# Performance work log

Hardware: AMD Instinct MI355X
Metric: run time of the kernel (lower is better)

Reference implementation:

```python
import jax, jax.numpy as jnp
import numpy as np

B, N, C, H = 4, 1024, 1024, 16
HD = C // H
SCALE = HD ** -0.5


def _init_linear(key, out_dim, in_dim):
    # torch nn.Linear default init: U(-1/sqrt(in), 1/sqrt(in)) for weight and bias
    kw, kb = jax.random.split(key)
    bound = 1.0 / np.sqrt(in_dim)
    W = jax.random.uniform(kw, (out_dim, in_dim), jnp.float32, -bound, bound)
    b = jax.random.uniform(kb, (out_dim,), jnp.float32, -bound, bound)
    return W, b


def setup_inputs() -> dict:
    key = jax.random.key(0)
    ks = jax.random.split(key, 5)
    x = jax.random.normal(ks[0], (B, N, C), jnp.float32)
    # NdLinear qkv: Linear(N->N) along seq axis, then Linear(C->3C) along channel axis
    Wq0, bq0 = _init_linear(ks[1], N, N)
    Wq1, bq1 = _init_linear(ks[2], 3 * C, C)
    # NdLinear proj: Linear(N->N) along seq axis, then Linear(C->C) along channel axis
    Wp0, bp0 = _init_linear(ks[3], N, N)
    Wp1, bp1 = _init_linear(ks[4], C, C)
    return {"x": x, "Wq0": Wq0, "bq0": bq0, "Wq1": Wq1, "bq1": bq1,
            "Wp0": Wp0, "bp0": bp0, "Wp1": Wp1, "bp1": bp1}


def _ndlinear(x, W0, b0, W1, b1):
    # NdLinear over (seq, channel): apply Linear along axis 1, then axis 2.
    # torch Linear: y = x @ W.T + b
    x = jnp.einsum('bnc,mn->bmc', x, W0) + b0[None, :, None]   # seq axis
    x = jnp.einsum('bnc,dc->bnd', x, W1) + b1                  # channel axis
    return x


def reference(x, Wq0, bq0, Wq1, bq1, Wp0, bp0, Wp1, bp1):
    qkv = _ndlinear(x, Wq0, bq0, Wq1, bq1)                     # (B, N, 3C)
    qkv = qkv.reshape(B, N, 3, H, HD).transpose(2, 0, 3, 1, 4) # (3, B, H, N, HD)
    q, k, v = qkv[0], qkv[1], qkv[2]
    attn = jnp.einsum('bhnd,bhmd->bhnm', q, k) * SCALE         # (B, H, N, N)
    attn = jax.nn.softmax(attn, axis=-1)
    out = jnp.einsum('bhnm,bhmd->bhnd', attn, v)               # (B, H, N, HD)
    out = out.transpose(0, 2, 1, 3).reshape(B, N, C)
    out = _ndlinear(out, Wp0, bp0, Wp1, bp1)
    return out
```

## Files before the change

### kernel.cpp

```cpp
#include <hip/hip_runtime.h>
#include <hip/hip_bf16.h>
#include <stdint.h>

typedef __bf16 bf16;
typedef __bf16 bf16x4 __attribute__((ext_vector_type(4)));
typedef __bf16 bf16x8 __attribute__((ext_vector_type(8)));
typedef float f32x4 __attribute__((ext_vector_type(4)));

#define B_ 4
#define N_ 1024
#define C_ 1024
#define H_ 16
#define MEG (1u << 20)

__device__ __forceinline__ uint32_t lds_off(const void* p) {
    return (uint32_t)(uintptr_t)p;
}
__device__ __forceinline__ void g2l16(const void* g, uint32_t lds_byte) {
    __builtin_amdgcn_global_load_lds(
        (const __attribute__((address_space(1))) unsigned int*)(uintptr_t)g,
        (__attribute__((address_space(3))) unsigned int*)(uintptr_t)lds_byte,
        16, 0, 0);
}

__global__ __launch_bounds__(256) void prep_k(
    const float* __restrict__ x, bf16* __restrict__ xT,
    const float* __restrict__ s0, bf16* __restrict__ d0,
    const float* __restrict__ s1, bf16* __restrict__ d1,
    const float* __restrict__ s2, bf16* __restrict__ d2,
    const float* __restrict__ s3, bf16* __restrict__ d3)
{
    __shared__ bf16 t[64][66];
    const int bid = blockIdx.x;
    const int tid = threadIdx.x;
    if (bid < 3072) {
        const float* s; bf16* d; int base;
        if (bid < 512)       { s = s0; d = d0; base = 0; }
        else if (bid < 2048) { s = s1; d = d1; base = 512; }
        else if (bid < 2560) { s = s2; d = d2; base = 2048; }
        else                 { s = s3; d = d3; base = 2560; }
        int i = ((bid - base) * 256 + tid) * 8;
        float4 a = *(const float4*)(s + i);
        float4 b = *(const float4*)(s + i + 4);
        bf16x8 r;
        r[0] = (bf16)a.x; r[1] = (bf16)a.y; r[2] = (bf16)a.z; r[3] = (bf16)a.w;
        r[4] = (bf16)b.x; r[5] = (bf16)b.y; r[6] = (bf16)b.z; r[7] = (bf16)b.w;
        *(bf16x8*)(d + i) = r;
        return;
    }
    const int idx = bid - 3072;
    const int c0 = (idx & 15) * 64, n0 = ((idx >> 4) & 15) * 64, b = idx >> 8;
    {
        int nl = tid >> 2, seg = tid & 3;
        const float* src = x + ((size_t)b * N_ + n0 + nl) * C_ + c0 + seg * 16;
#pragma unroll
        for (int i = 0; i < 4; ++i) {
            float4 v = *(const float4*)(src + i * 4);
            t[nl][seg * 16 + i * 4 + 0] = (bf16)v.x;
            t[nl][seg * 16 + i * 4 + 1] = (bf16)v.y;
            t[nl][seg * 16 + i * 4 + 2] = (bf16)v.z;
            t[nl][seg * 16 + i * 4 + 3] = (bf16)v.w;
        }
    }
    __syncthreads();
    {
        int cl = tid >> 2, seg = tid & 3;
        bf16* dst = xT + ((size_t)b * C_ + c0 + cl) * N_ + n0 + seg * 16;
        bf16x8 o0, o1;
#pragma unroll
        for (int j = 0; j < 8; ++j) o0[j] = t[seg * 16 + j][cl];
#pragma unroll
        for (int j = 0; j < 8; ++j) o1[j] = t[seg * 16 + 8 + j][cl];
        *(bf16x8*)dst = o0;
        *(bf16x8*)(dst + 8) = o1;
    }
}

template <int BIAS, bool OF32, bool VSPLIT>
__global__ __launch_bounds__(512) void gemm_k(
    const bf16* __restrict__ A, const bf16* __restrict__ Bm,
    const float* __restrict__ bias, void* __restrict__ Cv,
    bf16* __restrict__ vT,
    int M, int Nn, int K, long long sA, long long sB, long long sC)
{
    __shared__ bf16 smem[2][2][128 * 64];

    const int tid = threadIdx.x;
    const int lane = tid & 63, wid = tid >> 6;
    const int lr = lane & 15, lg = lane >> 4;
    const int wr = wid >> 2, wc = wid & 3;
    const int m0 = blockIdx.y * 128, n0 = blockIdx.x * 128;

    const bf16* Ab = A + (size_t)blockIdx.z * sA;
    const bf16* Bb = Bm + (size_t)blockIdx.z * sB;

    const uint32_t a_lds0 = lds_off(&smem[0][0][0]);
    const uint32_t b_lds0 = lds_off(&smem[0][1][0]);
    const uint32_t bufstride = 2 * 128 * 64 * 2;

    auto stage = [&](int kt, int buf) {
#pragma unroll
        for (int half = 0; half < 2; ++half) {
            int it = tid + half * 512;
            int r = it >> 3, ch = it & 7;
            int sch = ch ^ (r & 7);
            g2l16(Ab + (size_t)(m0 + r) * K + kt * 64 + sch * 8,
                  a_lds0 + buf * bufstride + it * 16);
            g2l16(Bb + (size_t)(n0 + r) * K + kt * 64 + sch * 8,
                  b_lds0 + buf * bufstride + it * 16);
        }
    };

    f32x4 acc[4][2];
#pragma unroll
    for (int i = 0; i < 4; ++i)
#pragma unroll
        for (int j = 0; j < 2; ++j) { f32x4 z = {0.f,0.f,0.f,0.f}; acc[i][j] = z; }

    stage(0, 0);
    __syncthreads();

    const int nt = K >> 6;
    for (int t = 0; t < nt; ++t) {
        int buf = t & 1;
        if (t + 1 < nt) stage(t + 1, buf ^ 1);
        const bf16* As = &smem[buf][0][0];
        const bf16* Bs = &smem[buf][1][0];
#pragma unroll
        for (int s = 0; s < 2; ++s) {
            bf16x8 af[4], bfr[2];
#pragma unroll
            for (int mi = 0; mi < 4; ++mi) {
                int row = wr * 64 + mi * 16 + lr;
                int slot = (s * 4 + lg) ^ (row & 7);
                af[mi] = *(const bf16x8*)(As + row * 64 + slot * 8);
            }
#pragma unroll
            for (int ni = 0; ni < 2; ++ni) {
                int row = wc * 32 + ni * 16 + lr;
                int slot = (s * 4 + lg) ^ (row & 7);
                bfr[ni] = *(const bf16x8*)(Bs + row * 64 + slot * 8);
            }
#pragma unroll
            for (int mi = 0; mi < 4; ++mi)
#pragma unroll
                for (int ni = 0; ni < 2; ++ni)
                    acc[mi][ni] = __builtin_amdgcn_mfma_f32_16x16x32_bf16(
                        af[mi], bfr[ni], acc[mi][ni], 0, 0, 0);
        }
        __syncthreads();
    }

#pragma unroll
    for (int mi = 0; mi < 4; ++mi)
#pragma unroll
        for (int ni = 0; ni < 2; ++ni) {
            int col = n0 + wc * 32 + ni * 16 + lr;
            if constexpr (VSPLIT) {
                if (col >= 2048) {
                    float bv = bias[col];
                    bf16x4 w;
#pragma unroll
                    for (int r = 0; r < 4; ++r) w[r] = (bf16)(acc[mi][ni][r] + bv);
                    int row0 = m0 + wr * 64 + mi * 16 + lg * 4;
                    int bb = row0 >> 10, n = row0 & 1023;
                    *(bf16x4*)(vT + (size_t)bb * MEG +
                               (size_t)(col - 2048) * 1024 + n) = w;
                    continue;
                }
            }
#pragma unroll
            for (int r = 0; r < 4; ++r) {
                int row = m0 + wr * 64 + mi * 16 + lg * 4 + r;
                float bv = (BIAS == 0) ? bias[row] : bias[col];
                float v = acc[mi][ni][r] + bv;
                if constexpr (OF32)
                    ((float*)Cv + (size_t)blockIdx.z * sC)[(size_t)row * Nn + col] = v;
                else
                    ((bf16*)Cv + (size_t)blockIdx.z * sC)[(size_t)row * Nn + col] = (bf16)v;
            }
        }
}

__global__ __launch_bounds__(256) void attn_k(
    const bf16* __restrict__ qkv, const bf16* __restrict__ vT,
    bf16* __restrict__ aoT)
{
    __shared__ bf16 Ks[2][4096];
    __shared__ bf16 Vs[2][4096];
    __shared__ bf16 pbuf[4][1024];

    const int tid = threadIdx.x;
    const int lane = tid & 63, wid = tid >> 6;
    const int lr = lane & 15, lg = lane >> 4;
    const int bid = blockIdx.x;
    const int qt = bid >> 6, hb = bid & 63;
    const int b = hb >> 4, h = hb & 15;
    const int qrow0 = qt * 64 + wid * 16;
    const int hoff = h * 64;
    const bf16* qkvb = qkv + (size_t)b * (N_ * 3 * C_);
    const bf16* vTb  = vT + (size_t)b * MEG;

    bf16x8 qf[2];
#pragma unroll
    for (int kk = 0; kk < 2; ++kk) {
        qf[kk] = *(const bf16x8*)(qkvb + (size_t)(qrow0 + lr) * 3072 +
                                  hoff + kk * 32 + lg * 8);
#pragma unroll
        for (int j = 0; j < 8; ++j)
            qf[kk][j] = (bf16)((float)qf[kk][j] * 0.18033688f);
    }

    const uint32_t ks0 = lds_off(&Ks[0][0]);
    const uint32_t vs0 = lds_off(&Vs[0][0]);

    auto stageK = [&](int kt, int buf) {
#pragma unroll
        for (int hh = 0; hh < 2; ++hh) {
            int it = tid + hh * 256;
            int key = it >> 3, ch = it & 7;
            int sch = ch ^ (key & 7);
            g2l16(qkvb + (size_t)(kt * 64 + key) * 3072 + C_ + hoff + sch * 8,
                  ks0 + buf * 8192 + it * 16);
        }
    };
    auto stageV = [&](int kt, int buf) {
#pragma unroll
        for (int hh = 0; hh < 2; ++hh) {
            int it = tid + hh * 256;
            int d = it >> 3, ch = it & 7;
            int sch = ch ^ (d & 7);
            g2l16(vTb + (size_t)(hoff + d) * 1024 + kt * 64 + sch * 8,
                  vs0 + buf * 8192 + it * 16);
        }
    };

    float lsum = 0.f;
    f32x4 o[4];
#pragma unroll
    for (int i = 0; i < 4; ++i) { f32x4 z = {0.f,0.f,0.f,0.f}; o[i] = z; }

    char* prow = (char*)&pbuf[wid][0] + lr * 128;
    const int swz = (lr & 7) << 4;

    stageK(0, 0);
    stageV(0, 0);
    __syncthreads();

    for (int kt = 0; kt < 16; ++kt) {
        int buf = kt & 1;
        if (kt + 1 < 16) {
            stageK(kt + 1, buf ^ 1);
            stageV(kt + 1, buf ^ 1);
        }

        f32x4 s[4];
        __builtin_amdgcn_s_setprio(1);
#pragma unroll
        for (int st = 0; st < 4; ++st) {
            f32x4 z = {0.f, 0.f, 0.f, 0.f};
#pragma unroll
            for (int kk = 0; kk < 2; ++kk) {
                int row = st * 16 + lr;
                int slot = (kk * 4 + lg) ^ (row & 7);
                bf16x8 kf = *(const bf16x8*)(&Ks[buf][row * 64 + slot * 8]);
                z = __builtin_amdgcn_mfma_f32_16x16x32_bf16(kf, qf[kk], z, 0, 0, 0);
            }
            s[st] = z;
        }
        __builtin_amdgcn_s_setprio(0);

#pragma unroll
        for (int st = 0; st < 4; ++st) {
            bf16x4 w;
#pragma unroll
            for (int r = 0; r < 4; ++r) {
                float e = __builtin_amdgcn_exp2f(s[st][r]);
                w[r] = (bf16)e;
                lsum += e;
            }
            *(bf16x4*)(prow + ((st * 32 + lg * 8) ^ swz)) = w;
        }

        bf16x8 pf[2];
        pf[0] = *(const bf16x8*)(prow + ((lg * 16) ^ swz));
        pf[1] = *(const bf16x8*)(prow + ((64 + lg * 16) ^ swz));

        __builtin_amdgcn_s_setprio(1);
#pragma unroll
        for (int dt = 0; dt < 4; ++dt) {
            int row = dt * 16 + lr;
            bf16x8 v0 = *(const bf16x8*)(&Vs[buf][row * 64 + ((lg ^ (lr & 7)) * 8)]);
            bf16x8 v1 = *(const bf16x8*)(&Vs[buf][row * 64 + (((4 + lg) ^ (lr & 7)) * 8)]);
            o[dt] = __builtin_amdgcn_mfma_f32_16x16x32_bf16(pf[0], v0, o[dt], 0, 0, 0);
            o[dt] = __builtin_amdgcn_mfma_f32_16x16x32_bf16(pf[1], v1, o[dt], 0, 0, 0);
        }
        __builtin_amdgcn_s_setprio(0);

        __syncthreads();
    }

    lsum += __shfl_xor(lsum, 16, 64);
    lsum += __shfl_xor(lsum, 32, 64);
    float rtot = 1.0f / lsum;
    float rcpo[4];
#pragma unroll
    for (int r = 0; r < 4; ++r) rcpo[r] = __shfl(rtot, lg * 4 + r, 64);

#pragma unroll
    for (int dt = 0; dt < 4; ++dt) {
        bf16x4 ov;
#pragma unroll
        for (int r = 0; r < 4; ++r) ov[r] = (bf16)(o[dt][r] * rcpo[r]);
        size_t c = (size_t)b * C_ + hoff + dt * 16 + lr;
        *(bf16x4*)(aoT + c * N_ + qrow0 + lg * 4) = ov;
    }
}

extern "C" void kernel_launch(void* const* d_in, const int* in_sizes, int n_in,
                              void* d_out, int out_size, void* d_ws, size_t ws_size,
                              hipStream_t stream) {
    (void)in_sizes; (void)n_in; (void)out_size; (void)ws_size;
    const float* x   = (const float*)d_in[0];
    const float* Wq0 = (const float*)d_in[1];
    const float* bq0 = (const float*)d_in[2];
    const float* Wq1 = (const float*)d_in[3];
    const float* bq1 = (const float*)d_in[4];
    const float* Wp0 = (const float*)d_in[5];
    const float* bp0 = (const float*)d_in[6];
    const float* Wp1 = (const float*)d_in[7];
    const float* bp1 = (const float*)d_in[8];

    bf16* ws   = (bf16*)d_ws;
    bf16* xT   = ws;
    bf16* Wq0b = ws + 4 * MEG;
    bf16* Wq1b = ws + 5 * MEG;
    bf16* Wp0b = ws + 8 * MEG;
    bf16* Wp1b = ws + 9 * MEG;
    bf16* y1   = ws + 10 * MEG;
    bf16* y2   = ws + 14 * MEG;
    bf16* vT   = xT;
    bf16* aoT  = y1;
    bf16* z1   = y2;
    float* outp = (float*)d_out;

    const long long s1M = (long long)N_ * C_;

    prep_k<<<dim3(4096), 256, 0, stream>>>(x, xT, Wq0, Wq0b, Wq1, Wq1b,
                                           Wp0, Wp0b, Wp1, Wp1b);

    gemm_k<0, false, false><<<dim3(8, 8, 4), 512, 0, stream>>>(
        Wq0b, xT, bq0, y1, nullptr, 1024, 1024, 1024, 0LL, s1M, s1M);
    gemm_k<1, false, true><<<dim3(24, 32, 1), 512, 0, stream>>>(
        y1, Wq1b, bq1, y2, vT, 4096, 3072, 1024, 0LL, 0LL, 0LL);
    attn_k<<<dim3(1024), 256, 0, stream>>>(y2, vT, aoT);
    gemm_k<0, false, false><<<dim3(8, 8, 4), 512, 0, stream>>>(
        Wp0b, aoT, bp0, z1, nullptr, 1024, 1024, 1024, 0LL, s1M, s1M);
    gemm_k<1, true, false><<<dim3(8, 32, 1), 512, 0, stream>>>(
        z1, Wp1b, bp1, outp, nullptr, 4096, 1024, 1024, 0LL, 0LL, 0LL);
}
```

Measured before the change: 119.9 us.

## Process two 16-row query tiles per wave in attention kernel

Each wave in the attention kernel now handles 32 query rows as two 16-row fragments, so every block covers 128 queries and the grid shrinks from 1024 to 512 blocks. Each K and V fragment read from LDS feeds two MFMAs, which halves the K/V global staging and LDS traffic per query and gives more independent MFMAs per iteration. The cost is roughly double the accumulator and score registers, a larger P buffer in LDS, and only 512 blocks on a many-CU device, which may hurt occupancy and load balance.

After: 118.6 us. Within noise of the previous version (-1.1%).

```diff
diff --git a/kernel.cpp b/kernel.cpp
--- a/kernel.cpp
+++ b/kernel.cpp
@@ -188,7 +188,7 @@
 {
     __shared__ bf16 Ks[2][4096];
     __shared__ bf16 Vs[2][4096];
-    __shared__ bf16 pbuf[4][1024];
+    __shared__ bf16 pbuf[4][2048];
 
     const int tid = threadIdx.x;
     const int lane = tid & 63, wid = tid >> 6;
@@ -196,19 +196,23 @@
     const int bid = blockIdx.x;
     const int qt = bid >> 6, hb = bid & 63;
     const int b = hb >> 4, h = hb & 15;
-    const int qrow0 = qt * 64 + wid * 16;
+    const int qrow0 = qt * 128 + wid * 32;
     const int hoff = h * 64;
     const bf16* qkvb = qkv + (size_t)b * (N_ * 3 * C_);
     const bf16* vTb  = vT + (size_t)b * MEG;
 
-    bf16x8 qf[2];
+    bf16x8 qfA[2], qfB[2];
 #pragma unroll
     for (int kk = 0; kk < 2; ++kk) {
-        qf[kk] = *(const bf16x8*)(qkvb + (size_t)(qrow0 + lr) * 3072 +
-                                  hoff + kk * 32 + lg * 8);
-#pragma unroll
-        for (int j = 0; j < 8; ++j)
-            qf[kk][j] = (bf16)((float)qf[kk][j] * 0.18033688f);
+        qfA[kk] = *(const bf16x8*)(qkvb + (size_t)(qrow0 + lr) * 3072 +
+                                   hoff + kk * 32 + lg * 8);
+        qfB[kk] = *(const bf16x8*)(qkvb + (size_t)(qrow0 + 16 + lr) * 3072 +
+                                   hoff + kk * 32 + lg * 8);
+#pragma unroll
+        for (int j = 0; j < 8; ++j) {
+            qfA[kk][j] = (bf16)((float)qfA[kk][j] * 0.18033688f);
+            qfB[kk][j] = (bf16)((float)qfB[kk][j] * 0.18033688f);
+        }
     }
 
     const uint32_t ks0 = lds_off(&Ks[0][0]);
@@ -235,12 +239,16 @@
         }
     };
 
-    float lsum = 0.f;
-    f32x4 o[4];
-#pragma unroll
-    for (int i = 0; i < 4; ++i) { f32x4 z = {0.f,0.f,0.f,0.f}; o[i] = z; }
-
-    char* prow = (char*)&pbuf[wid][0] + lr * 128;
+    float lsumA = 0.f, lsumB = 0.f;
+    f32x4 oA[4], oB[4];
+#pragma unroll
+    for (int i = 0; i < 4; ++i) {
+        f32x4 z = {0.f,0.f,0.f,0.f};
+        oA[i] = z; oB[i] = z;
+    }
+
+    char* prowA = (char*)&pbuf[wid][0] + lr * 128;
+    char* prowB = (char*)&pbuf[wid][0] + (16 + lr) * 128;
     const int swz = (lr & 7) << 4;
 
     stageK(0, 0);
@@ -254,37 +262,43 @@
             stageV(kt + 1, buf ^ 1);
         }
 
-        f32x4 s[4];
+        f32x4 sA[4], sB[4];
         __builtin_amdgcn_s_setprio(1);
 #pragma unroll
         for (int st = 0; st < 4; ++st) {
-            f32x4 z = {0.f, 0.f, 0.f, 0.f};
+            f32x4 zA = {0.f, 0.f, 0.f, 0.f};
+            f32x4 zB = {0.f, 0.f, 0.f, 0.f};
 #pragma unroll
             for (int kk = 0; kk < 2; ++kk) {
                 int row = st * 16 + lr;
                 int slot = (kk * 4 + lg) ^ (row & 7);
                 bf16x8 kf = *(const bf16x8*)(&Ks[buf][row * 64 + slot * 8]);
-                z = __builtin_amdgcn_mfma_f32_16x16x32_bf16(kf, qf[kk], z, 0, 0, 0);
-            }
-            s[st] = z;
+                zA = __builtin_amdgcn_mfma_f32_16x16x32_bf16(kf, qfA[kk], zA, 0, 0, 0);
+                zB = __builtin_amdgcn_mfma_f32_16x16x32_bf16(kf, qfB[kk], zB, 0, 0, 0);
+            }
+            sA[st] = zA; sB[st] = zB;
         }
         __builtin_amdgcn_s_setprio(0);
 
 #pragma unroll
         for (int st = 0; st < 4; ++st) {
-            bf16x4 w;
+            bf16x4 wA, wB;
 #pragma unroll
             for (int r = 0; r < 4; ++r) {
-                float e = __builtin_amdgcn_exp2f(s[st][r]);
-                w[r] = (bf16)e;
-                lsum += e;
-            }
-            *(bf16x4*)(prow + ((st * 32 + lg * 8) ^ swz)) = w;
-        }
-
-        bf16x8 pf[2];
-        pf[0] = *(const bf16x8*)(prow + ((lg * 16) ^ swz));
-        pf[1] = *(const bf16x8*)(prow + ((64 + lg * 16) ^ swz));
+                float eA = __builtin_amdgcn_exp2f(sA[st][r]);
+                float eB = __builtin_amdgcn_exp2f(sB[st][r]);
+                wA[r] = (bf16)eA; lsumA += eA;
+                wB[r] = (bf16)eB; lsumB += eB;
+            }
+            *(bf16x4*)(prowA + ((st * 32 + lg * 8) ^ swz)) = wA;
+            *(bf16x4*)(prowB + ((st * 32 + lg * 8) ^ swz)) = wB;
+        }
+
+        bf16x8 pfA[2], pfB[2];
+        pfA[0] = *(const bf16x8*)(prowA + ((lg * 16) ^ swz));
+        pfA[1] = *(const bf16x8*)(prowA + ((64 + lg * 16) ^ swz));
+        pfB[0] = *(const bf16x8*)(prowB + ((lg * 16) ^ swz));
+        pfB[1] = *(const bf16x8*)(prowB + ((64 + lg * 16) ^ swz));
 
         __builtin_amdgcn_s_setprio(1);
 #pragma unroll
@@ -292,28 +306,39 @@
             int row = dt * 16 + lr;
             bf16x8 v0 = *(const bf16x8*)(&Vs[buf][row * 64 + ((lg ^ (lr & 7)) * 8)]);
             bf16x8 v1 = *(const bf16x8*)(&Vs[buf][row * 64 + (((4 + lg) ^ (lr & 7)) * 8)]);
-            o[dt] = __builtin_amdgcn_mfma_f32_16x16x32_bf16(pf[0], v0, o[dt], 0, 0, 0);
-            o[dt] = __builtin_amdgcn_mfma_f32_16x16x32_bf16(pf[1], v1, o[dt], 0, 0, 0);
+            oA[dt] = __builtin_amdgcn_mfma_f32_16x16x32_bf16(pfA[0], v0, oA[dt], 0, 0, 0);
+            oA[dt] = __builtin_amdgcn_mfma_f32_16x16x32_bf16(pfA[1], v1, oA[dt], 0, 0, 0);
+            oB[dt] = __builtin_amdgcn_mfma_f32_16x16x32_bf16(pfB[0], v0, oB[dt], 0, 0, 0);
+            oB[dt] = __builtin_amdgcn_mfma_f32_16x16x32_bf16(pfB[1], v1, oB[dt], 0, 0, 0);
         }
         __builtin_amdgcn_s_setprio(0);
 
         __syncthreads();
     }
 
-    lsum += __shfl_xor(lsum, 16, 64);
-    lsum += __shfl_xor(lsum, 32, 64);
-    float rtot = 1.0f / lsum;
-    float rcpo[4];
-#pragma unroll
-    for (int r = 0; r < 4; ++r) rcpo[r] = __shfl(rtot, lg * 4 + r, 64);
+    lsumA += __shfl_xor(lsumA, 16, 64);
+    lsumA += __shfl_xor(lsumA, 32, 64);
+    lsumB += __shfl_xor(lsumB, 16, 64);
+    lsumB += __shfl_xor(lsumB, 32, 64);
+    float rtotA = 1.0f / lsumA, rtotB = 1.0f / lsumB;
+    float rcpoA[4], rcpoB[4];
+#pragma unroll
+    for (int r = 0; r < 4; ++r) {
+        rcpoA[r] = __shfl(rtotA, lg * 4 + r, 64);
+        rcpoB[r] = __shfl(rtotB, lg * 4 + r, 64);
+    }
 
 #pragma unroll
     for (int dt = 0; dt < 4; ++dt) {
-        bf16x4 ov;
-#pragma unroll
-        for (int r = 0; r < 4; ++r) ov[r] = (bf16)(o[dt][r] * rcpo[r]);
+        bf16x4 ovA, ovB;
+#pragma unroll
+        for (int r = 0; r < 4; ++r) {
+            ovA[r] = (bf16)(oA[dt][r] * rcpoA[r]);
+            ovB[r] = (bf16)(oB[dt][r] * rcpoB[r]);
+        }
         size_t c = (size_t)b * C_ + hoff + dt * 16 + lr;
-        *(bf16x4*)(aoT + c * N_ + qrow0 + lg * 4) = ov;
+        *(bf16x4*)(aoT + c * N_ + qrow0 + lg * 4) = ovA;
+        *(bf16x4*)(aoT + c * N_ + qrow0 + 16 + lg * 4) = ovB;
     }
 }
 
@@ -353,7 +378,7 @@
         Wq0b, xT, bq0, y1, nullptr, 1024, 1024, 1024, 0LL, s1M, s1M);
     gemm_k<1, false, true><<<dim3(24, 32, 1), 512, 0, stream>>>(
         y1, Wq1b, bq1, y2, vT, 4096, 3072, 1024, 0LL, 0LL, 0LL);
-    attn_k<<<dim3(1024), 256, 0, stream>>>(y2, vT, aoT);
+    attn_k<<<dim3(512), 256, 0, stream>>>(y2, vT, aoT);
     gemm_k<0, false, false><<<dim3(8, 8, 4), 512, 0, stream>>>(
         Wp0b, aoT, bp0, z1, nullptr, 1024, 1024, 1024, 0LL, s1M, s1M);
     gemm_k<1, true, false><<<dim3(8, 32, 1), 512, 0, stream>>>(
```
